# Optimization experiments

Measured on AMD Instinct MI355X. Metric: run time of the kernel, lower is better.

The kernel has to match this reference:

```python
import jax, jax.numpy as jnp
import numpy as np

B, S, DX, DM, H = 4, 2048, 1024, 1024, 16
DK = DM // H


def setup_inputs() -> dict:
    key = jax.random.key(0)
    ks = jax.random.split(key, 12)
    s = 0.02
    inp = {
        "q": jax.random.normal(ks[0], (B, S, DX), jnp.float32),
        "k": jax.random.normal(ks[1], (B, S, DX), jnp.float32),
        "v": jax.random.normal(ks[2], (B, S, DX), jnp.float32),
        "wq": jax.random.normal(ks[3], (DX, DM), jnp.float32) * s,
        "bq": jnp.zeros((DM,), jnp.float32),
        "wk": jax.random.normal(ks[4], (DX, DM), jnp.float32) * s,
        "bk": jnp.zeros((DM,), jnp.float32),
        "wv": jax.random.normal(ks[5], (DX, DM), jnp.float32) * s,
        "bv": jnp.zeros((DM,), jnp.float32),
        "wo": jax.random.normal(ks[6], (DM, DX), jnp.float32) * s,
        "bo": jnp.zeros((DX,), jnp.float32),
        # causal boolean mask [B, S_q, S_k]; True = attend
        "mask": jnp.broadcast_to(jnp.tril(jnp.ones((S, S), bool)), (B, S, S)),
    }
    return inp


def reference(q, k, v, wq, bq, wk, bk, wv, bv, wo, bo, mask):
    # Linear projections: [B,S,DX] @ [DX,DM] -> [B,S,DM]
    qh = (q @ wq + bq).reshape(B, S, H, DK).transpose(0, 2, 1, 3)  # [B,H,S,DK]
    kh = (k @ wk + bk).reshape(B, S, H, DK).transpose(0, 2, 1, 3)
    vh = (v @ wv + bv).reshape(B, S, H, DK).transpose(0, 2, 1, 3)

    scores = jnp.einsum("bhqd,bhkd->bhqk", qh, kh) / jnp.sqrt(jnp.float32(DK))
    neg = -jnp.finfo(scores.dtype).max
    scores = jnp.where(mask[:, None, :, :], scores, neg)  # mask.unsqueeze(1)
    p = jax.nn.softmax(scores, axis=-1)  # dropout inactive (eval / p=0)
    z = jnp.einsum("bhqk,bhkd->bhqd", p, vh)  # [B,H,S,DK]
    z = z.transpose(0, 2, 1, 3).reshape(B, S, DM)
    return z @ wo + bo
```

## Files before the change

kernel.cpp:

```cpp
#include <hip/hip_runtime.h>
#include <hip/hip_bf16.h>
#include <cstdint>

constexpr int Bb = 4, Sq = 2048, DXc = 1024, DMc = 1024, NH = 16, DKc = 64;
constexpr int GM = Bb * Sq;

typedef __attribute__((ext_vector_type(8))) short short8;
typedef __attribute__((ext_vector_type(4))) float f32x4;

__device__ inline unsigned short f2b(float f) {
  union { float f; uint32_t i; } c; c.f = f;
  uint32_t lsb = (c.i >> 16) & 1;
  c.i += 0x7fffu + lsb;
  return (unsigned short)(c.i >> 16);
}

__device__ inline uint32_t cvt_pk_bf16(float lo, float hi) {
  uint32_t r;
  asm("v_cvt_pk_bf16_f32 %0, %1, %2" : "=v"(r) : "v"(lo), "v"(hi));
  return r;
}

__device__ inline void load16_lds(const unsigned short* g, unsigned short* l) {
  __builtin_amdgcn_global_load_lds(
      (const __attribute__((address_space(1))) void*)g,
      (__attribute__((address_space(3))) void*)l, 16, 0, 0);
}

__global__ __launch_bounds__(256) void wt4_k(
    const float* __restrict__ wq, const float* __restrict__ wk,
    const float* __restrict__ wv, const float* __restrict__ wo,
    unsigned short* __restrict__ wqt, unsigned short* __restrict__ wkt,
    unsigned short* __restrict__ wvt, unsigned short* __restrict__ wot) {
  const int z = blockIdx.z;
  const float* W = z == 0 ? wq : z == 1 ? wk : z == 2 ? wv : wo;
  unsigned short* WT = z == 0 ? wqt : z == 1 ? wkt : z == 2 ? wvt : wot;
  __shared__ float t[64][65];
  const int tid = threadIdx.x;
  const int k0 = blockIdx.y * 64, n0 = blockIdx.x * 64;
#pragma unroll
  for (int p = 0; p < 4; ++p) {
    const int c = tid + p * 256;
    const int r = c >> 4, c4 = (c & 15) << 2;
    float4 v = *(const float4*)&W[(size_t)(k0 + r) * 1024 + n0 + c4];
    t[r][c4 + 0] = v.x; t[r][c4 + 1] = v.y; t[r][c4 + 2] = v.z; t[r][c4 + 3] = v.w;
  }
  __syncthreads();
#pragma unroll
  for (int p = 0; p < 4; ++p) {
    const int c = tid + p * 256;
    const int n = c >> 4, k4 = (c & 15) << 2;
    ushort4 o;
    o.x = f2b(t[k4 + 0][n]); o.y = f2b(t[k4 + 1][n]);
    o.z = f2b(t[k4 + 2][n]); o.w = f2b(t[k4 + 3][n]);
    *(ushort4*)&WT[(size_t)(n0 + n) * 1024 + k0 + k4] = o;
  }
}

__global__ __launch_bounds__(256) void qkv_k(
    const float* __restrict__ q, const float* __restrict__ k,
    const float* __restrict__ v,
    const unsigned short* __restrict__ wqt, const unsigned short* __restrict__ wkt,
    const unsigned short* __restrict__ wvt,
    const float* __restrict__ bq, const float* __restrict__ bk,
    const float* __restrict__ bv,
    unsigned short* __restrict__ qh, unsigned short* __restrict__ kh,
    unsigned short* __restrict__ vh) {
  constexpr int K = 1024;
  __shared__ __align__(16) unsigned short As[128 * 32];
  __shared__ __align__(16) unsigned short Bs[128 * 32];
  const int z = blockIdx.z;
  const float* A = z == 0 ? q : z == 1 ? k : v;
  const unsigned short* BT = z == 0 ? wqt : z == 1 ? wkt : wvt;
  const float* bias = z == 0 ? bq : z == 1 ? bk : bv;
  unsigned short* outB = z == 0 ? qh : z == 1 ? kh : vh;

  const int tid = threadIdx.x;
  const int lane = tid & 63;
  const int quad = lane >> 4, l16 = lane & 15;
  const int w = tid >> 6;
  const int wrow = (w >> 1) * 64, wcol = (w & 1) * 64;
  const int m0 = blockIdx.y * 128, n0 = blockIdx.x * 128;

  const int s0 = tid, s1 = tid + 256;
  const int ar0 = s0 >> 2, ac0 = (s0 & 3) * 8;
  const int ar1 = s1 >> 2, ac1 = (s1 & 3) * 8;

  f32x4 acc[4][4];
#pragma unroll
  for (int i = 0; i < 4; ++i)
#pragma unroll
    for (int j = 0; j < 4; ++j) acc[i][j] = (f32x4){0.f, 0.f, 0.f, 0.f};

  for (int k0 = 0; k0 < K; k0 += 32) {
    __syncthreads();
#pragma unroll
    for (int p = 0; p < 2; ++p) {
      const int c = tid + p * 256;
      const int row = c >> 2, ks = (c & 3) << 3;
      load16_lds(&BT[(size_t)(n0 + row) * K + k0 + ks], &Bs[c * 8]);
    }
    const float4 a0 = *(const float4*)&A[(size_t)(m0 + ar0) * K + k0 + ac0];
    const float4 a1 = *(const float4*)&A[(size_t)(m0 + ar0) * K + k0 + ac0 + 4];
    const float4 a2 = *(const float4*)&A[(size_t)(m0 + ar1) * K + k0 + ac1];
    const float4 a3 = *(const float4*)&A[(size_t)(m0 + ar1) * K + k0 + ac1 + 4];
    {
      uint4 p0, p1;
      p0.x = cvt_pk_bf16(a0.x, a0.y); p0.y = cvt_pk_bf16(a0.z, a0.w);
      p0.z = cvt_pk_bf16(a1.x, a1.y); p0.w = cvt_pk_bf16(a1.z, a1.w);
      p1.x = cvt_pk_bf16(a2.x, a2.y); p1.y = cvt_pk_bf16(a2.z, a2.w);
      p1.z = cvt_pk_bf16(a3.x, a3.y); p1.w = cvt_pk_bf16(a3.z, a3.w);
      *(uint4*)&As[s0 * 8] = p0;
      *(uint4*)&As[s1 * 8] = p1;
    }
    __syncthreads();

    short8 af[4], bf[4];
#pragma unroll
    for (int i = 0; i < 4; ++i)
      af[i] = *(const short8*)&As[(wrow + i * 16 + l16) * 32 + quad * 8];
#pragma unroll
    for (int j = 0; j < 4; ++j)
      bf[j] = *(const short8*)&Bs[(wcol + j * 16 + l16) * 32 + quad * 8];
#pragma unroll
    for (int i = 0; i < 4; ++i)
#pragma unroll
      for (int j = 0; j < 4; ++j)
        acc[i][j] = __builtin_amdgcn_mfma_f32_16x16x32_bf16(af[i], bf[j], acc[i][j], 0, 0, 0);
  }

  float bvv[4];
#pragma unroll
  for (int j = 0; j < 4; ++j) bvv[j] = bias[n0 + wcol + j * 16 + l16];
#pragma unroll
  for (int i = 0; i < 4; ++i)
#pragma unroll
    for (int j = 0; j < 4; ++j)
#pragma unroll
      for (int r = 0; r < 4; ++r) {
        const int m = m0 + wrow + i * 16 + quad * 4 + r;
        const int n = n0 + wcol + j * 16 + l16;
        const float val = acc[i][j][r] + bvv[j];
        const int b = m >> 11, s = m & 2047, h = n >> 6, d = n & 63;
        if (z < 2) {
          outB[(((size_t)(b * NH + h) * Sq + s) << 6) + d] = f2b(val);
        } else {
          outB[(((size_t)(b * NH + h) * DKc + d) << 11) + s] = f2b(val);
        }
      }
}

__global__ __launch_bounds__(256) void mgemm_o(
    const unsigned short* __restrict__ A, const unsigned short* __restrict__ BT,
    const float* __restrict__ bias, float* __restrict__ outF) {
  constexpr int K = 1024;
  __shared__ __align__(16) unsigned short As[128 * 32];
  __shared__ __align__(16) unsigned short Bs[128 * 32];
  const int tid = threadIdx.x;
  const int lane = tid & 63;
  const int quad = lane >> 4, l16 = lane & 15;
  const int w = tid >> 6;
  const int wrow = (w >> 1) * 64, wcol = (w & 1) * 64;
  const int m0 = blockIdx.y * 128, n0 = blockIdx.x * 128;

  f32x4 acc[4][4];
#pragma unroll
  for (int i = 0; i < 4; ++i)
#pragma unroll
    for (int j = 0; j < 4; ++j) acc[i][j] = (f32x4){0.f, 0.f, 0.f, 0.f};

  for (int k0 = 0; k0 < K; k0 += 32) {
    __syncthreads();
#pragma unroll
    for (int p = 0; p < 2; ++p) {
      const int c = tid + p * 256;
      const int row = c >> 2, ks = (c & 3) << 3;
      load16_lds(&A[(size_t)(m0 + row) * K + k0 + ks], &As[c * 8]);
      load16_lds(&BT[(size_t)(n0 + row) * K + k0 + ks], &Bs[c * 8]);
    }
    __syncthreads();

    short8 af[4], bf[4];
#pragma unroll
    for (int i = 0; i < 4; ++i)
      af[i] = *(const short8*)&As[(wrow + i * 16 + l16) * 32 + quad * 8];
#pragma unroll
    for (int j = 0; j < 4; ++j)
      bf[j] = *(const short8*)&Bs[(wcol + j * 16 + l16) * 32 + quad * 8];
#pragma unroll
    for (int i = 0; i < 4; ++i)
#pragma unroll
      for (int j = 0; j < 4; ++j)
        acc[i][j] = __builtin_amdgcn_mfma_f32_16x16x32_bf16(af[i], bf[j], acc[i][j], 0, 0, 0);
  }

  float bv[4];
#pragma unroll
  for (int j = 0; j < 4; ++j) bv[j] = bias[n0 + wcol + j * 16 + l16];
#pragma unroll
  for (int i = 0; i < 4; ++i)
#pragma unroll
    for (int j = 0; j < 4; ++j)
#pragma unroll
      for (int r = 0; r < 4; ++r) {
        const int m = m0 + wrow + i * 16 + quad * 4 + r;
        const int n = n0 + wcol + j * 16 + l16;
        outF[(size_t)m * 1024 + n] = acc[i][j][r] + bv[j];
      }
}

__global__ __launch_bounds__(512) void flash_k(
    const unsigned short* __restrict__ Qh, const unsigned short* __restrict__ Kh,
    const unsigned short* __restrict__ Vt, unsigned short* __restrict__ Zb) {
  constexpr int LDP = 72;
  __shared__ __align__(16) unsigned short Klds[64 * 64];
  __shared__ __align__(16) unsigned short Vlds[64 * 64];
  __shared__ __align__(16) unsigned short Plds[8 * 16 * LDP];
  const int tid = threadIdx.x;
  const int w = tid >> 6, lane = tid & 63;
  const int quad = lane >> 4, l16 = lane & 15;
  const int bh = blockIdx.x & 63;
  const int qi = blockIdx.x >> 6;
  const int qa = qi * 128;
  const int qbv = (15 - qi) * 128;
  const size_t base = (size_t)bh * Sq * DKc;
  unsigned short* Pw = &Plds[w * 16 * LDP];

  const int qb[2] = {qa + w * 16, qbv + (7 - w) * 16};
  const int tiles_s[2] = {2 * qi + 1 + (w >= 4 ? 1 : 0),
                          31 - 2 * qi + (w < 4 ? 1 : 0)};
  const int ntile = 32 - 2 * qi;

  short8 qf0[2], qf1[2];
#pragma unroll
  for (int s = 0; s < 2; ++s) {
    const unsigned short* qp = Qh + base + (size_t)(qb[s] + l16) * DKc + quad * 8;
    qf0[s] = *(const short8*)qp;
    qf1[s] = *(const short8*)(qp + 32);
  }

  f32x4 oacc[2][4];
#pragma unroll
  for (int s = 0; s < 2; ++s)
#pragma unroll
    for (int n = 0; n < 4; ++n) oacc[s][n] = (f32x4){0.f, 0.f, 0.f, 0.f};
  float lsum[2] = {0.f, 0.f};

  const int row0 = tid >> 3, sp0 = tid & 7;
  const int xseg = sp0 ^ (row0 & 7);
  const int dst = (row0 * 8 + xseg) * 8;
  const int pos0 = quad ^ (l16 & 7);
  const int pos1 = pos0 ^ 4;

  uint4 kreg = *(const uint4*)(Kh + base + (size_t)row0 * DKc + sp0 * 8);
  uint4 vreg = *(const uint4*)(Vt + base + (size_t)row0 * Sq + sp0 * 8);

  for (int it = 0; it < ntile; ++it) {
    const int kt0 = it * 64;
    __syncthreads();
    *(uint4*)&Klds[dst] = kreg;
    *(uint4*)&Vlds[dst] = vreg;
    if (it + 1 < ntile) {
      const int kn = kt0 + 64;
      kreg = *(const uint4*)(Kh + base + (size_t)(kn + row0) * DKc + sp0 * 8);
      vreg = *(const uint4*)(Vt + base + (size_t)row0 * Sq + kn + sp0 * 8);
    }
    __syncthreads();

    short8 kf0[4], kf1[4];
#pragma unroll
    for (int t = 0; t < 4; ++t) {
      const int krow = (t * 16 + l16) * 64;
      kf0[t] = *(const short8*)&Klds[krow + pos0 * 8];
      kf1[t] = *(const short8*)&Klds[krow + pos1 * 8];
    }

#pragma unroll
    for (int s = 0; s < 2; ++s) {
      if (it >= tiles_s[s]) continue;
      f32x4 st[4];
#pragma unroll
      for (int t = 0; t < 4; ++t) {
        f32x4 z4 = (f32x4){0.f, 0.f, 0.f, 0.f};
        z4 = __builtin_amdgcn_mfma_f32_16x16x32_bf16(kf0[t], qf0[s], z4, 0, 0, 0);
        st[t] = __builtin_amdgcn_mfma_f32_16x16x32_bf16(kf1[t], qf1[s], z4, 0, 0, 0);
      }
      const int qrow = qb[s] + l16;
      float p[4][4];
      if (it == tiles_s[s] - 1) {
#pragma unroll
        for (int t = 0; t < 4; ++t)
#pragma unroll
          for (int r = 0; r < 4; ++r) {
            const int key = kt0 + t * 16 + quad * 4 + r;
            const float e = __expf(fminf(st[t][r] * 0.125f, 30.f));
            p[t][r] = (key <= qrow) ? e : 0.f;
          }
      } else {
#pragma unroll
        for (int t = 0; t < 4; ++t)
#pragma unroll
          for (int r = 0; r < 4; ++r)
            p[t][r] = __expf(fminf(st[t][r] * 0.125f, 30.f));
      }
#pragma unroll
      for (int t = 0; t < 4; ++t)
#pragma unroll
        for (int r = 0; r < 4; ++r) lsum[s] += p[t][r];
#pragma unroll
      for (int t = 0; t < 4; ++t) {
        ushort4 pk;
        pk.x = f2b(p[t][0]); pk.y = f2b(p[t][1]);
        pk.z = f2b(p[t][2]); pk.w = f2b(p[t][3]);
        *(ushort4*)&Pw[l16 * LDP + t * 16 + quad * 4] = pk;
      }
      short8 pf0 = *(const short8*)&Pw[l16 * LDP + quad * 8];
      short8 pf1 = *(const short8*)&Pw[l16 * LDP + 32 + quad * 8];
#pragma unroll
      for (int n = 0; n < 4; ++n) {
        const int vrow = (n * 16 + l16) * 64;
        short8 vf0 = *(const short8*)&Vlds[vrow + pos0 * 8];
        short8 vf1 = *(const short8*)&Vlds[vrow + pos1 * 8];
        oacc[s][n] = __builtin_amdgcn_mfma_f32_16x16x32_bf16(pf0, vf0, oacc[s][n], 0, 0, 0);
        oacc[s][n] = __builtin_amdgcn_mfma_f32_16x16x32_bf16(pf1, vf1, oacc[s][n], 0, 0, 0);
      }
    }
  }

  const int b = bh >> 4, h = bh & 15;
#pragma unroll
  for (int s = 0; s < 2; ++s) {
    float ls = lsum[s];
    ls += __shfl_xor(ls, 16, 64);
    ls += __shfl_xor(ls, 32, 64);
    const float inv = 1.f / ls;
    float invr[4];
#pragma unroll
    for (int r = 0; r < 4; ++r) invr[r] = __shfl(inv, quad * 4 + r, 64);
#pragma unroll
    for (int r = 0; r < 4; ++r) {
      const int row = qb[s] + quad * 4 + r;
      unsigned short* zp = Zb + ((size_t)b * Sq + row) * DMc + h * 64;
#pragma unroll
      for (int n = 0; n < 4; ++n) zp[n * 16 + l16] = f2b(oacc[s][n][r] * invr[r]);
    }
  }
}

extern "C" void kernel_launch(void* const* d_in, const int* in_sizes, int n_in,
                              void* d_out, int out_size, void* d_ws, size_t ws_size,
                              hipStream_t stream) {
  const float* q  = (const float*)d_in[0];
  const float* k  = (const float*)d_in[1];
  const float* v  = (const float*)d_in[2];
  const float* wq = (const float*)d_in[3];
  const float* bq = (const float*)d_in[4];
  const float* wk = (const float*)d_in[5];
  const float* bk = (const float*)d_in[6];
  const float* wv = (const float*)d_in[7];
  const float* bv = (const float*)d_in[8];
  const float* wo = (const float*)d_in[9];
  const float* bo = (const float*)d_in[10];

  constexpr size_t NEL = (size_t)GM * DMc;
  unsigned short* qh  = (unsigned short*)d_ws;
  unsigned short* kh  = qh + NEL;
  unsigned short* vh  = kh + NEL;
  unsigned short* xbf = vh + NEL;
  unsigned short* wqt = xbf + NEL;
  unsigned short* wkt = wqt + (size_t)DXc * DMc;
  unsigned short* wvt = wkt + (size_t)DXc * DMc;
  unsigned short* wot = wvt + (size_t)DXc * DMc;

  wt4_k<<<dim3(16, 16, 4), 256, 0, stream>>>(wq, wk, wv, wo, wqt, wkt, wvt, wot);
  qkv_k<<<dim3(8, 64, 3), 256, 0, stream>>>(q, k, v, wqt, wkt, wvt,
                                            bq, bk, bv, qh, kh, vh);
  flash_k<<<dim3(512), 512, 0, stream>>>(qh, kh, vh, xbf);
  mgemm_o<<<dim3(8, 64), 256, 0, stream>>>(xbf, wot, bo, (float*)d_out);
}
```

Measured before the change: 395.2 us.

## Remap GEMM blocks per XCD and load flash K/V tiles directly to LDS

```diff
diff --git a/kernel.cpp b/kernel.cpp
--- a/kernel.cpp
+++ b/kernel.cpp
@@ -25,6 +25,12 @@
   __builtin_amdgcn_global_load_lds(
       (const __attribute__((address_space(1))) void*)g,
       (__attribute__((address_space(3))) void*)l, 16, 0, 0);
+}
+
+__device__ inline void xcd_map(int d, int& m0, int& n0) {
+  const int c = d & 7, k = d >> 3;
+  n0 = (k & 7) * 128;
+  m0 = (c * 8 + (k >> 3)) * 128;
 }
 
 __global__ __launch_bounds__(256) void wt4_k(
@@ -69,7 +75,7 @@
   constexpr int K = 1024;
   __shared__ __align__(16) unsigned short As[128 * 32];
   __shared__ __align__(16) unsigned short Bs[128 * 32];
-  const int z = blockIdx.z;
+  const int z = blockIdx.y;
   const float* A = z == 0 ? q : z == 1 ? k : v;
   const unsigned short* BT = z == 0 ? wqt : z == 1 ? wkt : wvt;
   const float* bias = z == 0 ? bq : z == 1 ? bk : bv;
@@ -80,7 +86,8 @@
   const int quad = lane >> 4, l16 = lane & 15;
   const int w = tid >> 6;
   const int wrow = (w >> 1) * 64, wcol = (w & 1) * 64;
-  const int m0 = blockIdx.y * 128, n0 = blockIdx.x * 128;
+  int m0, n0;
+  xcd_map(blockIdx.x, m0, n0);
 
   const int s0 = tid, s1 = tid + 256;
   const int ar0 = s0 >> 2, ac0 = (s0 & 3) * 8;
@@ -161,7 +168,8 @@
   const int quad = lane >> 4, l16 = lane & 15;
   const int w = tid >> 6;
   const int wrow = (w >> 1) * 64, wcol = (w & 1) * 64;
-  const int m0 = blockIdx.y * 128, n0 = blockIdx.x * 128;
+  int m0, n0;
+  xcd_map(blockIdx.x, m0, n0);
 
   f32x4 acc[4][4];
 #pragma unroll
@@ -246,25 +254,15 @@
     for (int n = 0; n < 4; ++n) oacc[s][n] = (f32x4){0.f, 0.f, 0.f, 0.f};
   float lsum[2] = {0.f, 0.f};
 
-  const int row0 = tid >> 3, sp0 = tid & 7;
-  const int xseg = sp0 ^ (row0 & 7);
-  const int dst = (row0 * 8 + xseg) * 8;
+  const int row0 = tid >> 3, sp0 = tid & 7, gs0 = sp0 ^ (row0 & 7);
   const int pos0 = quad ^ (l16 & 7);
   const int pos1 = pos0 ^ 4;
 
-  uint4 kreg = *(const uint4*)(Kh + base + (size_t)row0 * DKc + sp0 * 8);
-  uint4 vreg = *(const uint4*)(Vt + base + (size_t)row0 * Sq + sp0 * 8);
-
   for (int it = 0; it < ntile; ++it) {
     const int kt0 = it * 64;
     __syncthreads();
-    *(uint4*)&Klds[dst] = kreg;
-    *(uint4*)&Vlds[dst] = vreg;
-    if (it + 1 < ntile) {
-      const int kn = kt0 + 64;
-      kreg = *(const uint4*)(Kh + base + (size_t)(kn + row0) * DKc + sp0 * 8);
-      vreg = *(const uint4*)(Vt + base + (size_t)row0 * Sq + kn + sp0 * 8);
-    }
+    load16_lds(Kh + base + (size_t)(kt0 + row0) * DKc + gs0 * 8, &Klds[tid * 8]);
+    load16_lds(Vt + base + (size_t)row0 * Sq + kt0 + gs0 * 8, &Vlds[tid * 8]);
     __syncthreads();
 
     short8 kf0[4], kf1[4];
@@ -373,8 +371,8 @@
   unsigned short* wot = wvt + (size_t)DXc * DMc;
 
   wt4_k<<<dim3(16, 16, 4), 256, 0, stream>>>(wq, wk, wv, wo, wqt, wkt, wvt, wot);
-  qkv_k<<<dim3(8, 64, 3), 256, 0, stream>>>(q, k, v, wqt, wkt, wvt,
-                                            bq, bk, bv, qh, kh, vh);
+  qkv_k<<<dim3(512, 3), 256, 0, stream>>>(q, k, v, wqt, wkt, wvt,
+                                          bq, bk, bv, qh, kh, vh);
   flash_k<<<dim3(512), 512, 0, stream>>>(qh, kh, vh, xbf);
-  mgemm_o<<<dim3(8, 64), 256, 0, stream>>>(xbf, wot, bo, (float*)d_out);
-}
+  mgemm_o<<<dim3(512), 256, 0, stream>>>(xbf, wot, bo, (float*)d_out);
+}
```

Measured after the change: 410.1 us. +3.8%, slower.
